# Optimization experiments

Hardware: AMD Instinct MI355X
Metric: run time of the kernel (lower is better)

## Reference

```python
import jax, jax.numpy as jnp
import numpy as np

WINDOW_SIZES = [3, 5, 7, 9]
THETA = 1.0
INCLUDE = ['contrast', 'energy', 'entropy', 'homogeneity']
EPS = 1e-6


def _extract_patches(x, w):
    # x: [B, C, H, W] -> [B, C, K=w*w, H, W] with zero padding (matches F.unfold)
    pad = w // 2
    H, W = x.shape[2], x.shape[3]
    xp = jnp.pad(x, ((0, 0), (0, 0), (pad, pad), (pad, pad)))
    shifts = [xp[:, :, i:i + H, j:j + W] for i in range(w) for j in range(w)]
    return jnp.stack(shifts, axis=2)


def _glcm_feats(patches):
    # patches: [B, C, K, H, W]; all reductions over K (axis=2)
    mean = jnp.mean(patches, axis=2, keepdims=True)
    std = jnp.std(patches, axis=2, ddof=1, keepdims=True) + EPS  # torch.std is unbiased
    normed = (patches - mean) / std
    contrast = jnp.mean(normed ** 2, axis=2)
    energy = jnp.mean(patches ** 2, axis=2)
    entropy = -jnp.mean(patches * jnp.log(patches + EPS), axis=2)
    homogeneity = 1.0 / jnp.mean(1.0 + jnp.abs(patches - mean), axis=2)
    return {'contrast': contrast, 'energy': energy,
            'entropy': entropy, 'homogeneity': homogeneity}


def setup_inputs() -> dict:
    key = jax.random.key(0)
    x = jax.random.uniform(key, (2, 3, 512, 512), dtype=jnp.float32)
    return {'x': x}


def reference(x):
    B, C, H, W = x.shape
    per_window = []
    for w in WINDOW_SIZES:
        patches = _extract_patches(x, w)          # [B, C, K, H, W]
        feats = _glcm_feats(patches)
        Ms = []
        for name in ['contrast', 'energy', 'entropy', 'homogeneity']:
            if name in INCLUDE:
                log_feat = jnp.log(feats[name] + EPS)
                Ms.append(jnp.exp(THETA * log_feat - 0.5 * THETA ** 2))
        per_window.append(jnp.stack(Ms, axis=2))  # [B, C, F, H, W]
    out = jnp.concatenate(per_window, axis=2)     # [B, C, nW*F, H, W]
    # channel-major ordering (c outer, then window, then feature) matches the
    # torch module's per-channel loop + final cat along dim=1
    return out.reshape(B, C * out.shape[2], H, W)
```

## Files before the change

### kernel.cpp

```cpp
#include <hip/hip_runtime.h>
#include <math.h>

#define BC 6
#define H_ 512
#define W_ 512
#define HW (H_ * W_)
#define EPS 1e-6f
#define EXPM05 0.60653065971263342f

#define TW 72
#define TH 24
#define XSS 26
#define VHS 72

__global__ __launch_bounds__(512) void texmart_kernel(const float* __restrict__ x,
                                                      float* __restrict__ out) {
    __shared__ float xs[TW][XSS];
    __shared__ float vh[48][VHS];

    const int tx = threadIdx.x, ty = threadIdx.y;
    const int tid = ty * 64 + tx;
    const int bx = blockIdx.x * 64, by = blockIdx.y * 16;
    const int plane = blockIdx.z;
    const float* __restrict__ xp = x + (size_t)plane * HW;

    for (int idx = tid; idx < TW * TH; idx += 512) {
        const int t = idx / TW, c = idx - t * TW;
        const int gy = by + t - 4, gx = bx + c - 4;
        float v = 0.f;
        if (gy >= 0 && gy < H_ && gx >= 0 && gx < W_) v = xp[gy * W_ + gx];
        xs[c][t] = v;
    }
    __syncthreads();

    int uoA[3], ucA[3];
    float s1A[3], s2A[3], slA[3];
#pragma unroll
    for (int i = 0; i < 3; ++i) {
        const int u = tid + i * 512;
        const int uu = (u < 1152) ? u : 0;
        const int o = uu / 72, c = uu - o * 72;
        uoA[i] = o; ucA[i] = c;
        const float pc = xs[c][o + 4];
        s1A[i] = pc;
        s2A[i] = pc * pc;
        slA[i] = pc * __logf(pc + EPS);
    }

    float mean[2][4];
    const int gxx = bx + tx;
    float* __restrict__ obase = out + (size_t)plane * 16 * HW + (size_t)by * W_ + gxx;

#pragma unroll
    for (int R = 1; R <= 4; ++R) {
#pragma unroll
        for (int i = 0; i < 3; ++i) {
            if (i < 2 || tid < 128) {
                const int o = uoA[i], c = ucA[i];
                const float plo = xs[c][o + 4 - R];
                const float phi = xs[c][o + 4 + R];
                s1A[i] += plo + phi;
                s2A[i] = __fmaf_rn(plo, plo, __fmaf_rn(phi, phi, s2A[i]));
                slA[i] += plo * __logf(plo + EPS) + phi * __logf(phi + EPS);
                vh[o][c]      = s1A[i];
                vh[16 + o][c] = s2A[i];
                vh[32 + o][c] = slA[i];
            }
        }
        __syncthreads();

        const float K = (float)((2 * R + 1) * (2 * R + 1));
        const float invK = 1.f / K;
        const float invKm1 = 1.f / (K - 1.f);
#pragma unroll
        for (int oi = 0; oi < 2; ++oi) {
            const int o = ty * 2 + oi;
            float S1 = 0.f, S2 = 0.f, SL = 0.f;
#pragma unroll
            for (int s = -4; s <= 4; ++s) {
                if (s >= -R && s <= R) {
                    S1 += vh[o][tx + 4 + s];
                    S2 += vh[16 + o][tx + 4 + s];
                    SL += vh[32 + o][tx + 4 + s];
                }
            }
            const float m = S1 * invK;
            mean[oi][R - 1] = m;
            float S2c = __fmaf_rn(-S1, m, S2);
            if (S2c < 0.f) S2c = 0.f;
            const float sd = sqrtf(S2c * invKm1) + EPS;
            const float contrast = (S2c * invK) * __frcp_rn(sd * sd);
            const float energy = S2 * invK;
            const float entropy = -SL * invK;

            float* __restrict__ o4 = obase + (size_t)o * W_ + (size_t)(R - 1) * 4 * HW;
            o4[0 * HW] = (contrast + EPS) * EXPM05;
            o4[1 * HW] = (energy + EPS) * EXPM05;
            o4[2 * HW] = (entropy + EPS) * EXPM05;
        }
        if (R < 4) __syncthreads();
    }

    const int ty2 = ty * 2;
    float sa[2][4];
#pragma unroll
    for (int oi = 0; oi < 2; ++oi)
#pragma unroll
        for (int R = 0; R < 4; ++R) sa[oi][R] = 0.f;

#pragma unroll
    for (int dj = 0; dj < 9; ++dj) {
        const int a = dj < 4 ? 4 - dj : dj - 4;
        const float* __restrict__ col = &xs[tx + dj][ty2];
        const float2 u0 = *(const float2*)(col + 0);
        const float2 u1 = *(const float2*)(col + 2);
        const float2 u2 = *(const float2*)(col + 4);
        const float2 u3 = *(const float2*)(col + 6);
        const float2 u4 = *(const float2*)(col + 8);
        const float p[10] = {u0.x, u0.y, u1.x, u1.y, u2.x, u2.y, u3.x, u3.y, u4.x, u4.y};

#pragma unroll
        for (int oi = 0; oi < 2; ++oi) {
#pragma unroll
            for (int k = 0; k < 9; ++k) {
                const int adi = k < 4 ? 4 - k : k - 4;
                const int rm = a > adi ? a : adi;
                const int r0 = rm < 1 ? 1 : rm;
#pragma unroll
                for (int R = 1; R <= 4; ++R) {
                    if (R >= r0) sa[oi][R - 1] += fabsf(p[oi + k] - mean[oi][R - 1]);
                }
            }
        }
    }

#pragma unroll
    for (int oi = 0; oi < 2; ++oi) {
        const int o = ty2 + oi;
#pragma unroll
        for (int R = 1; R <= 4; ++R) {
            const float K = (float)((2 * R + 1) * (2 * R + 1));
            const float homog = __frcp_rn(1.f + sa[oi][R - 1] * (1.f / K));
            obase[(size_t)o * W_ + (size_t)(R - 1) * 4 * HW + 3 * HW] =
                (homog + EPS) * EXPM05;
        }
    }
}

extern "C" void kernel_launch(void* const* d_in, const int* in_sizes, int n_in,
                              void* d_out, int out_size, void* d_ws, size_t ws_size,
                              hipStream_t stream) {
    const float* x = (const float*)d_in[0];
    float* out = (float*)d_out;
    dim3 block(64, 8, 1);
    dim3 grid(W_ / 64, H_ / 16, BC);
    texmart_kernel<<<grid, block, 0, stream>>>(x, out);
}
```

Baseline: 42.75 us.

## Store vertical window sums as packed half2 and precompute p·log(p) once

The kernel now computes p·log(p) once per tile element into a second shared array, instead of recomputing the log for every radius. The vertical partial sums for all four radii are built in one pass and stored as packed fp16 half2 pairs, one per two output rows. This replaces the per-radius write/sync/read rounds with a single barrier, and the horizontal sums use __hadd2 on half2. The cost is accuracy: sums of up to 81 terms and the variance computed as S2 − S1·mean are done in fp16, which risks large errors in contrast from cancellation.

```diff
diff --git a/kernel.cpp b/kernel.cpp
--- a/kernel.cpp
+++ b/kernel.cpp
@@ -1,4 +1,5 @@
 #include <hip/hip_runtime.h>
+#include <hip/hip_fp16.h>
 #include <math.h>
 
 #define BC 6
@@ -11,12 +12,12 @@
 #define TW 72
 #define TH 24
 #define XSS 26
-#define VHS 72
 
 __global__ __launch_bounds__(512) void texmart_kernel(const float* __restrict__ x,
                                                       float* __restrict__ out) {
     __shared__ float xs[TW][XSS];
-    __shared__ float vh[48][VHS];
+    __shared__ float qs[TW][XSS];
+    __shared__ __half2 vh[12][8][72];
 
     const int tx = threadIdx.x, ty = threadIdx.y;
     const int tid = ty * 64 + tx;
@@ -30,22 +31,35 @@
         float v = 0.f;
         if (gy >= 0 && gy < H_ && gx >= 0 && gx < W_) v = xp[gy * W_ + gx];
         xs[c][t] = v;
+        qs[c][t] = v * __logf(v + EPS);
     }
     __syncthreads();
 
-    int uoA[3], ucA[3];
-    float s1A[3], s2A[3], slA[3];
+    __half* __restrict__ vhh = (__half*)vh;
 #pragma unroll
     for (int i = 0; i < 3; ++i) {
-        const int u = tid + i * 512;
-        const int uu = (u < 1152) ? u : 0;
-        const int o = uu / 72, c = uu - o * 72;
-        uoA[i] = o; ucA[i] = c;
-        const float pc = xs[c][o + 4];
-        s1A[i] = pc;
-        s2A[i] = pc * pc;
-        slA[i] = pc * __logf(pc + EPS);
+        if (i < 2 || tid < 128) {
+            const int u = tid + i * 512;
+            const int o = u / 72, c = u - (u / 72) * 72;
+            float s1 = xs[c][o + 4];
+            float s2 = s1 * s1;
+            float sl = qs[c][o + 4];
+            const int wbase = (o >> 1) * 72 + c;
+            const int half = o & 1;
+#pragma unroll
+            for (int R = 1; R <= 4; ++R) {
+                const float plo = xs[c][o + 4 - R];
+                const float phi = xs[c][o + 4 + R];
+                s1 += plo + phi;
+                s2 = __fmaf_rn(plo, plo, __fmaf_rn(phi, phi, s2));
+                sl += qs[c][o + 4 - R] + qs[c][o + 4 + R];
+                vhh[2 * (((0 * 4 + R - 1) * 8 * 72) + wbase) + half] = __float2half(s1);
+                vhh[2 * (((1 * 4 + R - 1) * 8 * 72) + wbase) + half] = __float2half(s2);
+                vhh[2 * (((2 * 4 + R - 1) * 8 * 72) + wbase) + half] = __float2half(sl);
+            }
+        }
     }
+    __syncthreads();
 
     float mean[2][4];
     const int gxx = bx + tx;
@@ -53,21 +67,20 @@
 
 #pragma unroll
     for (int R = 1; R <= 4; ++R) {
+        __half2 a1 = __float2half2_rn(0.f);
+        __half2 a2 = __float2half2_rn(0.f);
+        __half2 al = __float2half2_rn(0.f);
 #pragma unroll
-        for (int i = 0; i < 3; ++i) {
-            if (i < 2 || tid < 128) {
-                const int o = uoA[i], c = ucA[i];
-                const float plo = xs[c][o + 4 - R];
-                const float phi = xs[c][o + 4 + R];
-                s1A[i] += plo + phi;
-                s2A[i] = __fmaf_rn(plo, plo, __fmaf_rn(phi, phi, s2A[i]));
-                slA[i] += plo * __logf(plo + EPS) + phi * __logf(phi + EPS);
-                vh[o][c]      = s1A[i];
-                vh[16 + o][c] = s2A[i];
-                vh[32 + o][c] = slA[i];
+        for (int s = -4; s <= 4; ++s) {
+            if (s >= -R && s <= R) {
+                a1 = __hadd2(a1, vh[0 * 4 + R - 1][ty][tx + 4 + s]);
+                a2 = __hadd2(a2, vh[1 * 4 + R - 1][ty][tx + 4 + s]);
+                al = __hadd2(al, vh[2 * 4 + R - 1][ty][tx + 4 + s]);
             }
         }
-        __syncthreads();
+        const float S1v[2] = {__low2float(a1), __high2float(a1)};
+        const float S2v[2] = {__low2float(a2), __high2float(a2)};
+        const float SLv[2] = {__low2float(al), __high2float(al)};
 
         const float K = (float)((2 * R + 1) * (2 * R + 1));
         const float invK = 1.f / K;
@@ -75,30 +88,20 @@
 #pragma unroll
         for (int oi = 0; oi < 2; ++oi) {
             const int o = ty * 2 + oi;
-            float S1 = 0.f, S2 = 0.f, SL = 0.f;
-#pragma unroll
-            for (int s = -4; s <= 4; ++s) {
-                if (s >= -R && s <= R) {
-                    S1 += vh[o][tx + 4 + s];
-                    S2 += vh[16 + o][tx + 4 + s];
-                    SL += vh[32 + o][tx + 4 + s];
-                }
-            }
-            const float m = S1 * invK;
+            const float m = S1v[oi] * invK;
             mean[oi][R - 1] = m;
-            float S2c = __fmaf_rn(-S1, m, S2);
+            float S2c = __fmaf_rn(-S1v[oi], m, S2v[oi]);
             if (S2c < 0.f) S2c = 0.f;
             const float sd = sqrtf(S2c * invKm1) + EPS;
             const float contrast = (S2c * invK) * __frcp_rn(sd * sd);
-            const float energy = S2 * invK;
-            const float entropy = -SL * invK;
+            const float energy = S2v[oi] * invK;
+            const float entropy = -SLv[oi] * invK;
 
             float* __restrict__ o4 = obase + (size_t)o * W_ + (size_t)(R - 1) * 4 * HW;
             o4[0 * HW] = (contrast + EPS) * EXPM05;
             o4[1 * HW] = (energy + EPS) * EXPM05;
             o4[2 * HW] = (entropy + EPS) * EXPM05;
         }
-        if (R < 4) __syncthreads();
     }
 
     const int ty2 = ty * 2;
```

New measurement: 41.62 us. -2.6%, faster.
